# Performance work log

Hardware: AMD Instinct MI355X
Metric: run time of the kernel (lower is better)

Reference implementation:

```python
import jax, jax.numpy as jnp
import numpy as np

BLOCK = 8
HALO = 3
HEADS = 4


def setup_inputs() -> dict:
    key = jax.random.key(0)
    ks = jax.random.split(key, 8)
    B, C, H, W = 4, 256, 128, 128
    d = C // HEADS
    win = BLOCK + 2 * HALO
    s = lambda k, shape, scale=1.0: jax.random.normal(k, shape, jnp.float32) * scale
    return {
        'noisy': s(ks[0], (B, C, H, W)),
        'aux': s(ks[1], (B, C, H, W)),
        'w_map': s(ks[2], (C, 2 * C), (2.0 / (2 * C)) ** 0.5),  # 1x1 conv: [out, in]
        'b_map': jnp.zeros((C,), jnp.float32),
        'w_q': s(ks[3], (C, C), (2.0 / C) ** 0.5),
        'w_k': s(ks[4], (C, C), (2.0 / C) ** 0.5),
        'w_v': s(ks[5], (C, C), (2.0 / C) ** 0.5),
        'rel_h': s(ks[6], (win, 1, d // 2)),
        'rel_w': s(ks[7], (1, win, d // 2)),
    }


def _conv1x1(x, w):
    # x: [B,C,H,W], w: [O,C]
    return jnp.einsum('oc,bchw->bohw', w, x)


def reference(noisy, aux, w_map, b_map, w_q, w_k, w_v, rel_h, rel_w):
    B, C, H, W = noisy.shape
    block, halo, heads = BLOCK, HALO, HEADS
    d = C // heads
    win = block + 2 * halo
    nbh, nbw = H // block, W // block

    n_aux = jax.nn.relu(_conv1x1(jnp.concatenate([noisy, aux], axis=1), w_map)
                        + b_map[None, :, None, None])

    # Q: [B,nbh,nbw,heads,block*block,d], pre-scaled by head_ch**-0.5
    q = _conv1x1(n_aux, w_q) * (d ** -0.5)
    q = q.reshape(B, heads, d, nbh, block, nbw, block)
    q = q.transpose(0, 3, 5, 1, 4, 6, 2).reshape(B, nbh, nbw, heads, block * block, d)

    def halo_windows(x):
        xp = jnp.pad(x, ((0, 0), (0, 0), (halo, halo), (halo, halo)))
        ih = jnp.arange(nbh)[:, None] * block + jnp.arange(win)[None, :]
        iw = jnp.arange(nbw)[:, None] * block + jnp.arange(win)[None, :]
        w1 = xp[:, :, ih, :]
        w2 = w1[:, :, :, :, iw]
        w2 = w2.transpose(0, 2, 4, 1, 3, 5)
        w2 = w2.reshape(B, nbh, nbw, heads, d, win, win)
        return w2.transpose(0, 1, 2, 3, 5, 6, 4)

    k = halo_windows(_conv1x1(n_aux, w_k))
    # relative position bias fused into K (first half: height, second half: width)
    k = jnp.concatenate([k[..., :d // 2] + rel_h, k[..., d // 2:] + rel_w], axis=-1)
    k = k.reshape(B, nbh, nbw, heads, win * win, d)

    v = halo_windows(_conv1x1(noisy, w_v)).reshape(B, nbh, nbw, heads, win * win, d)

    sim = jnp.einsum('bxyhid,bxyhjd->bxyhij', q, k)
    attn = jax.nn.softmax(sim, axis=-1)
    out = jnp.einsum('bxyhij,bxyhjd->bxyhid', attn, v)

    # reassemble blocks: [B,nbh,nbw,heads,block,block,d] -> [B, heads*d, H, W]
    out = out.reshape(B, nbh, nbw, heads, block, block, d)
    out = out.transpose(0, 3, 6, 1, 4, 2, 5).reshape(B, C, H, W)
    return out
```

## Files before the change

kernel.cpp:

```cpp
#include <hip/hip_runtime.h>
#include <hip/hip_bf16.h>

typedef unsigned short u16;
typedef __attribute__((ext_vector_type(8))) short short8;
typedef __attribute__((ext_vector_type(4))) float floatx4;

#define HWPIX 16384
#define IMG 128

__device__ __forceinline__ float b2f(u16 u) {
    unsigned int x = ((unsigned int)u) << 16;
    return __builtin_bit_cast(float, x);
}
__device__ __forceinline__ u16 f2b(float f) {
    __hip_bfloat16 h = __float2bfloat16(f);
    return __builtin_bit_cast(u16, h);
}

template<int IN_WS>
__global__ __launch_bounds__(256)
void conv1x1_kernel(const float* __restrict__ ein0, const float* __restrict__ ein1,
                    const u16* __restrict__ bws,
                    const float* __restrict__ w, const float* __restrict__ bias,
                    u16* __restrict__ out, int K, float scale, int relu)
{
    __shared__ u16 Alds[64 * 40];
    __shared__ u16 Blds[128 * 40];

    const int tid = threadIdx.x;
    const int wave = tid >> 6, lane = tid & 63;
    const int quad = lane >> 4, l16 = lane & 15;
    const int pbase = blockIdx.x * 128;
    const int mbase = blockIdx.y * 64;
    const int b = blockIdx.z;

    floatx4 acc[8];
#pragma unroll
    for (int f = 0; f < 8; ++f) acc[f] = (floatx4){0.f, 0.f, 0.f, 0.f};

    const int a_r = tid >> 2, a_kg = tid & 3;
    const int b_c4 = (tid & 7) * 4;
    const int b_p4 = (tid >> 3) * 4;

    float4 af0, af1;
    float4 bfl[4];
    uint2  bbl[4];

    auto load_chunk = [&](int kc) {
        const int c0 = kc * 32;
        const float* wp = w + (size_t)(mbase + a_r) * K + c0 + a_kg * 8;
        af0 = *(const float4*)wp;
        af1 = *(const float4*)(wp + 4);
        if (IN_WS) {
#pragma unroll
            for (int i = 0; i < 4; ++i) {
                const u16* s = bws + ((size_t)b * 256 + c0 + b_c4 + i) * HWPIX + pbase + b_p4;
                bbl[i] = *(const uint2*)s;
            }
        } else {
            const float* base = (c0 < 256) ? ein0 : ein1;
            const int cb = c0 & 255;
#pragma unroll
            for (int i = 0; i < 4; ++i) {
                const float* s = base + ((size_t)b * 256 + cb + b_c4 + i) * HWPIX + pbase + b_p4;
                bfl[i] = *(const float4*)s;
            }
        }
    };
    auto write_chunk = [&]() {
        union { uint4 v; u16 s[8]; } ta;
        ta.s[0] = f2b(af0.x); ta.s[1] = f2b(af0.y); ta.s[2] = f2b(af0.z); ta.s[3] = f2b(af0.w);
        ta.s[4] = f2b(af1.x); ta.s[5] = f2b(af1.y); ta.s[6] = f2b(af1.z); ta.s[7] = f2b(af1.w);
        *(uint4*)&Alds[a_r * 40 + a_kg * 8] = ta.v;
        if (IN_WS) {
            union { uint2 v; u16 s[4]; } c[4];
#pragma unroll
            for (int i = 0; i < 4; ++i) c[i].v = bbl[i];
#pragma unroll
            for (int j = 0; j < 4; ++j) {
                union { uint2 v; u16 s[4]; } o;
#pragma unroll
                for (int i = 0; i < 4; ++i) o.s[i] = c[i].s[j];
                *(uint2*)&Blds[(b_p4 + j) * 40 + b_c4] = o.v;
            }
        } else {
            float px[4][4];
#pragma unroll
            for (int i = 0; i < 4; ++i) {
                px[i][0] = bfl[i].x; px[i][1] = bfl[i].y; px[i][2] = bfl[i].z; px[i][3] = bfl[i].w;
            }
#pragma unroll
            for (int j = 0; j < 4; ++j) {
                union { uint2 v; u16 s[4]; } o;
#pragma unroll
                for (int i = 0; i < 4; ++i) o.s[i] = f2b(px[i][j]);
                *(uint2*)&Blds[(b_p4 + j) * 40 + b_c4] = o.v;
            }
        }
    };

    const int nchunk = K >> 5;
    load_chunk(0);
    for (int kc = 0; kc < nchunk; ++kc) {
        if (kc) __syncthreads();
        write_chunk();
        __syncthreads();
        if (kc + 1 < nchunk) load_chunk(kc + 1);
        short8 afrag = *(const short8*)&Alds[(wave * 16 + l16) * 40 + quad * 8];
#pragma unroll
        for (int f = 0; f < 8; ++f) {
            short8 bfrag = *(const short8*)&Blds[(f * 16 + l16) * 40 + quad * 8];
            acc[f] = __builtin_amdgcn_mfma_f32_16x16x32_bf16(afrag, bfrag, acc[f], 0, 0, 0);
        }
    }

    float bv[4];
#pragma unroll
    for (int r = 0; r < 4; ++r) {
        int m = mbase + wave * 16 + quad * 4 + r;
        bv[r] = bias ? bias[m] : 0.f;
    }
#pragma unroll
    for (int f = 0; f < 8; ++f) {
        int p = pbase + f * 16 + l16;
#pragma unroll
        for (int r = 0; r < 4; ++r) {
            int m = mbase + wave * 16 + quad * 4 + r;
            float v = acc[f][r] * scale + bv[r];
            if (relu) v = fmaxf(v, 0.f);
            out[((size_t)b * 256 + m) * HWPIX + p] = f2b(v);
        }
    }
}

__global__ __launch_bounds__(256)
void attn_kernel(const u16* __restrict__ qmap, const u16* __restrict__ kmap,
                 const u16* __restrict__ vmap, const float* __restrict__ relh,
                 const float* __restrict__ relw, float* __restrict__ out)
{
    __shared__ u16 Qlds[64 * 72];
    __shared__ u16 Klds[224 * 72];
    __shared__ u16 Vlds[64 * 232];
    __shared__ float RelHf[448], RelWf[448];

    const int tid = threadIdx.x;
    const int wave = tid >> 6, lane = tid & 63;
    const int quad = lane >> 4, l16 = lane & 15;

    const int n = blockIdx.x + 16 * blockIdx.y + 256 * blockIdx.z;
    const int n2 = (n & 7) * 512 + (n >> 3);
    const int bw = n2 & 15, bh = (n2 >> 4) & 15;
    const int head = (n2 >> 8) & 3, b = n2 >> 10;

    const size_t chbase = ((size_t)b * 256 + head * 64) * HWPIX;

    float rh0 = relh[tid], rw0 = relw[tid];
    float rh1 = 0.f, rw1 = 0.f;
    if (tid < 192) { rh1 = relh[tid + 256]; rw1 = relw[tid + 256]; }

    const u16* qrow = qmap + chbase + (size_t)lane * HWPIX + bw * 8;
    uint4 q0 = *(const uint4*)(qrow + (bh * 8 + wave) * IMG);
    uint4 q1 = *(const uint4*)(qrow + (bh * 8 + wave + 4) * IMG);

    const int cbyte = min(max(bw * 16 - 8, 0), 224);
    uint2 kseg[4][4], vseg[4][4];
#pragma unroll
    for (int s = 0; s < 4; ++s) {
        if (s < 3 || wave < 2) {
            const int wr = wave + 4 * s;
            const int ih = bh * 8 - 3 + wr;
            const int ihc = min(max(ih, 0), 127);
            const char* kp = (const char*)(kmap + chbase + (size_t)lane * HWPIX) + ihc * 256 + cbyte;
            const char* vp = (const char*)(vmap + chbase + (size_t)lane * HWPIX) + ihc * 256 + cbyte;
#pragma unroll
            for (int j = 0; j < 4; ++j) {
                kseg[s][j] = *(const uint2*)(kp + 8 * j);
                vseg[s][j] = *(const uint2*)(vp + 8 * j);
            }
        }
    }

    RelHf[tid] = rh0; RelWf[tid] = rw0;
    if (tid < 192) { RelHf[tid + 256] = rh1; RelWf[tid + 256] = rw1; }
    {
        union { uint4 v; u16 s[8]; } t0, t1;
        t0.v = q0; t1.v = q1;
#pragma unroll
        for (int i = 0; i < 8; ++i) {
            Qlds[(wave * 8 + i) * 72 + lane] = t0.s[i];
            Qlds[((wave + 4) * 8 + i) * 72 + lane] = t1.s[i];
        }
    }
    __syncthreads();

    const int iwb = bw * 8 - 3;
#pragma unroll
    for (int s = 0; s < 4; ++s) {
        if (s < 3 || wave < 2) {
            const int wr = wave + 4 * s;
            const int ih = bh * 8 - 3 + wr;
            const bool rok = (unsigned)ih < 128u;
            union { uint2 v[4]; u16 u[16]; } kr, vr;
#pragma unroll
            for (int j = 0; j < 4; ++j) { kr.v[j] = kseg[s][j]; vr.v[j] = vseg[s][j]; }
            if (bw == 0) {
#pragma unroll
                for (int i = 15; i >= 4; --i) { kr.u[i] = kr.u[i - 4]; vr.u[i] = vr.u[i - 4]; }
            } else if (bw == 15) {
#pragma unroll
                for (int i = 0; i < 12; ++i) { kr.u[i] = kr.u[i + 4]; vr.u[i] = vr.u[i + 4]; }
            }
            const int kb = wr * 14;
            u16 vm[14];
#pragma unroll
            for (int sc = 0; sc < 14; ++sc) {
                const bool ok = rok && ((unsigned)(iwb + sc) < 128u);
                vm[sc] = ok ? vr.u[sc + 1] : (u16)0;
                const float kv = ok ? b2f(kr.u[sc + 1]) : 0.f;
                const float rel = (lane < 32) ? RelHf[wr * 32 + (lane & 31)]
                                              : RelWf[sc * 32 + (lane & 31)];
                Klds[(kb + sc) * 72 + lane] = f2b(kv + rel);
            }
            unsigned* vrow = (unsigned*)&Vlds[lane * 232 + kb];
#pragma unroll
            for (int p = 0; p < 7; ++p)
                vrow[p] = (unsigned)vm[2 * p] | ((unsigned)vm[2 * p + 1] << 16);
        }
    }
    for (int t = tid; t < 28 * 64; t += 256) {
        int kp_ = 196 + (t >> 6), ch = t & 63;
        Klds[kp_ * 72 + ch] = 0;
        Vlds[ch * 232 + kp_] = 0;
    }
    __syncthreads();

    floatx4 sacc[14];
#pragma unroll
    for (int f = 0; f < 14; ++f) sacc[f] = (floatx4){0.f, 0.f, 0.f, 0.f};
    __builtin_amdgcn_s_setprio(1);
#pragma unroll
    for (int kc = 0; kc < 2; ++kc) {
        short8 qa = *(const short8*)&Qlds[(wave * 16 + l16) * 72 + kc * 32 + quad * 8];
#pragma unroll
        for (int f = 0; f < 14; ++f) {
            short8 kb = *(const short8*)&Klds[(f * 16 + l16) * 72 + kc * 32 + quad * 8];
            sacc[f] = __builtin_amdgcn_mfma_f32_16x16x32_bf16(qa, kb, sacc[f], 0, 0, 0);
        }
    }
    __builtin_amdgcn_s_setprio(0);

    float pm[14][4], rmax[4], rsum[4];
#pragma unroll
    for (int r = 0; r < 4; ++r) rmax[r] = -3.0e4f;
#pragma unroll
    for (int f = 0; f < 14; ++f) {
        int col = f * 16 + l16;
#pragma unroll
        for (int r = 0; r < 4; ++r) {
            float v = (col < 196) ? sacc[f][r] : -3.0e4f;
            pm[f][r] = v;
            rmax[r] = fmaxf(rmax[r], v);
        }
    }
#pragma unroll
    for (int off = 1; off < 16; off <<= 1)
#pragma unroll
        for (int r = 0; r < 4; ++r)
            rmax[r] = fmaxf(rmax[r], __shfl_xor(rmax[r], off, 64));
#pragma unroll
    for (int r = 0; r < 4; ++r) rsum[r] = 0.f;
#pragma unroll
    for (int f = 0; f < 14; ++f)
#pragma unroll
        for (int r = 0; r < 4; ++r) {
            float e = __expf(pm[f][r] - rmax[r]);
            pm[f][r] = e;
            rsum[r] += e;
        }
#pragma unroll
    for (int off = 1; off < 16; off <<= 1)
#pragma unroll
        for (int r = 0; r < 4; ++r)
            rsum[r] += __shfl_xor(rsum[r], off, 64);
    float rinv[4];
#pragma unroll
    for (int r = 0; r < 4; ++r) rinv[r] = 1.f / rsum[r];

    __syncthreads();

    u16* S = Klds;
#pragma unroll
    for (int f = 0; f < 14; ++f)
#pragma unroll
        for (int r = 0; r < 4; ++r)
            S[(wave * 16 + quad * 4 + r) * 232 + f * 16 + l16] = f2b(pm[f][r] * rinv[r]);
    __syncthreads();

    floatx4 oacc[4];
#pragma unroll
    for (int f = 0; f < 4; ++f) oacc[f] = (floatx4){0.f, 0.f, 0.f, 0.f};
    __builtin_amdgcn_s_setprio(1);
#pragma unroll
    for (int kc = 0; kc < 7; ++kc) {
        short8 pa = *(const short8*)&S[(wave * 16 + l16) * 232 + kc * 32 + quad * 8];
#pragma unroll
        for (int f = 0; f < 4; ++f) {
            short8 vb = *(const short8*)&Vlds[(f * 16 + l16) * 232 + kc * 32 + quad * 8];
            oacc[f] = __builtin_amdgcn_mfma_f32_16x16x32_bf16(pa, vb, oacc[f], 0, 0, 0);
        }
    }
    __builtin_amdgcn_s_setprio(0);

    u16* O = Qlds;
#pragma unroll
    for (int f = 0; f < 4; ++f)
#pragma unroll
        for (int r = 0; r < 4; ++r)
            O[(f * 16 + l16) * 72 + wave * 16 + quad * 4 + r] = f2b(oacc[f][r]);
    __syncthreads();

    for (int t = tid; t < 512; t += 256) {
        int ch = t >> 3, r = t & 7;
        const u16* src = &O[ch * 72 + r * 8];
        float4 v0 = {b2f(src[0]), b2f(src[1]), b2f(src[2]), b2f(src[3])};
        float4 v1 = {b2f(src[4]), b2f(src[5]), b2f(src[6]), b2f(src[7])};
        float* dst = out + chbase + ch * HWPIX + (bh * 8 + r) * IMG + bw * 8;
        *(float4*)dst = v0;
        *(float4*)(dst + 4) = v1;
    }
}

extern "C" void kernel_launch(void* const* d_in, const int* in_sizes, int n_in,
                              void* d_out, int out_size, void* d_ws, size_t ws_size,
                              hipStream_t stream)
{
    (void)in_sizes; (void)n_in; (void)out_size; (void)ws_size;
    const float* noisy = (const float*)d_in[0];
    const float* aux   = (const float*)d_in[1];
    const float* w_map = (const float*)d_in[2];
    const float* b_map = (const float*)d_in[3];
    const float* w_q   = (const float*)d_in[4];
    const float* w_k   = (const float*)d_in[5];
    const float* w_v   = (const float*)d_in[6];
    const float* rel_h = (const float*)d_in[7];
    const float* rel_w = (const float*)d_in[8];
    float* out = (float*)d_out;

    u16* nv   = (u16*)d_ws;
    u16* kmap = nv   + (size_t)16777216;
    u16* qmap = kmap + (size_t)16777216;

    dim3 cgrid(128, 4, 4);
    conv1x1_kernel<0><<<cgrid, 256, 0, stream>>>(noisy, aux, nullptr, w_map, b_map, nv,   512, 1.f,    1);
    conv1x1_kernel<1><<<cgrid, 256, 0, stream>>>(nullptr, nullptr, nv, w_q,  nullptr, qmap, 256, 0.125f, 0);
    conv1x1_kernel<1><<<cgrid, 256, 0, stream>>>(nullptr, nullptr, nv, w_k,  nullptr, kmap, 256, 1.f,    0);
    conv1x1_kernel<0><<<cgrid, 256, 0, stream>>>(noisy, noisy, nullptr, w_v, nullptr, nv,   256, 1.f,    0);
    attn_kernel<<<dim3(16, 16, 16), 256, 0, stream>>>(qmap, kmap, nv, rel_h, rel_w, out);
}
```

Before: 430.8 us.

## Pre-convert weights to bf16, enlarge conv tiles, fuse Q/K convs, swizzle V LDS

Adds a kernel that converts all 1x1 conv weights to bf16 in a device global buffer, so the conv kernels no longer convert weights per tile. The conv kernel's tile grows to 128x128 outputs with a 64-wide K chunk, and each wave now computes a 4x4 grid of MFMA fragments for more reuse per LDS load. The Q and K projections are merged into a single launch by splitting on blockIdx.y. In the attention kernel, the V LDS layout becomes a 512-byte-row XOR swizzle to avoid bank conflicts. The trade-off is higher register and LDS use per block, which may lower occupancy, plus one extra small launch.

```diff
diff --git a/kernel.cpp b/kernel.cpp
--- a/kernel.cpp
+++ b/kernel.cpp
@@ -17,120 +17,157 @@
     return __builtin_bit_cast(u16, h);
 }
 
+__device__ __align__(16) u16 g_w16[327680];
+
+__global__ __launch_bounds__(256)
+void wconv_kernel(const float* __restrict__ wmap, const float* __restrict__ wq,
+                  const float* __restrict__ wk, const float* __restrict__ wv)
+{
+    int i = blockIdx.x * 256 + threadIdx.x;
+    const float* src; int off;
+    if (i < 131072)      { src = wmap; off = i; }
+    else if (i < 196608) { src = wk;   off = i - 131072; }
+    else if (i < 262144) { src = wq;   off = i - 196608; }
+    else                 { src = wv;   off = i - 262144; }
+    g_w16[i] = f2b(src[off]);
+}
+
 template<int IN_WS>
 __global__ __launch_bounds__(256)
-void conv1x1_kernel(const float* __restrict__ ein0, const float* __restrict__ ein1,
-                    const u16* __restrict__ bws,
-                    const float* __restrict__ w, const float* __restrict__ bias,
-                    u16* __restrict__ out, int K, float scale, int relu)
+void conv2_kernel(const float* __restrict__ ein0, const float* __restrict__ ein1,
+                  const u16* __restrict__ bws, int woff,
+                  const float* __restrict__ bias,
+                  u16* __restrict__ outA, u16* __restrict__ outB,
+                  int K, float scaleA, float scaleB, int relu)
 {
-    __shared__ u16 Alds[64 * 40];
-    __shared__ u16 Blds[128 * 40];
+    __shared__ u16 Alds[128 * 72];
+    __shared__ u16 Blds[128 * 72];
 
     const int tid = threadIdx.x;
     const int wave = tid >> 6, lane = tid & 63;
     const int quad = lane >> 4, l16 = lane & 15;
+    const int wmo = (wave >> 1) * 64;
+    const int wpo = (wave & 1) * 64;
     const int pbase = blockIdx.x * 128;
-    const int mbase = blockIdx.y * 64;
+    const int mbase = blockIdx.y * 128;
     const int b = blockIdx.z;
-
-    floatx4 acc[8];
-#pragma unroll
-    for (int f = 0; f < 8; ++f) acc[f] = (floatx4){0.f, 0.f, 0.f, 0.f};
-
-    const int a_r = tid >> 2, a_kg = tid & 3;
-    const int b_c4 = (tid & 7) * 4;
-    const int b_p4 = (tid >> 3) * 4;
-
-    float4 af0, af1;
-    float4 bfl[4];
-    uint2  bbl[4];
+    u16* out = (blockIdx.y >= 2) ? outB : outA;
+    const float scale = (blockIdx.y >= 2) ? scaleB : scaleA;
+    const int mb = mbase & 255;
+    const u16* wsrc = g_w16 + woff;
+
+    floatx4 acc[4][4];
+#pragma unroll
+    for (int mi = 0; mi < 4; ++mi)
+#pragma unroll
+        for (int pj = 0; pj < 4; ++pj) acc[mi][pj] = (floatx4){0.f, 0.f, 0.f, 0.f};
+
+    const int a_r = tid >> 1, a_s = (tid & 1) * 32;
+    const int b_c = (tid & 15) * 4;
+    const int b_p = (tid >> 4) * 8;
+
+    uint4  apre[4];
+    uint4  bpre[4];
+    float4 fpre[4][2];
 
     auto load_chunk = [&](int kc) {
-        const int c0 = kc * 32;
-        const float* wp = w + (size_t)(mbase + a_r) * K + c0 + a_kg * 8;
-        af0 = *(const float4*)wp;
-        af1 = *(const float4*)(wp + 4);
+        const int c0 = kc * 64;
+        const u16* wp = wsrc + (size_t)(mbase + a_r) * K + c0 + a_s;
+#pragma unroll
+        for (int j = 0; j < 4; ++j) apre[j] = *(const uint4*)(wp + j * 8);
         if (IN_WS) {
 #pragma unroll
-            for (int i = 0; i < 4; ++i) {
-                const u16* s = bws + ((size_t)b * 256 + c0 + b_c4 + i) * HWPIX + pbase + b_p4;
-                bbl[i] = *(const uint2*)s;
-            }
+            for (int i = 0; i < 4; ++i)
+                bpre[i] = *(const uint4*)(bws + ((size_t)b * 256 + c0 + b_c + i) * HWPIX + pbase + b_p);
         } else {
             const float* base = (c0 < 256) ? ein0 : ein1;
             const int cb = c0 & 255;
 #pragma unroll
             for (int i = 0; i < 4; ++i) {
-                const float* s = base + ((size_t)b * 256 + cb + b_c4 + i) * HWPIX + pbase + b_p4;
-                bfl[i] = *(const float4*)s;
+                const float* s = base + ((size_t)b * 256 + cb + b_c + i) * HWPIX + pbase + b_p;
+                fpre[i][0] = *(const float4*)s;
+                fpre[i][1] = *(const float4*)(s + 4);
             }
         }
     };
     auto write_chunk = [&]() {
-        union { uint4 v; u16 s[8]; } ta;
-        ta.s[0] = f2b(af0.x); ta.s[1] = f2b(af0.y); ta.s[2] = f2b(af0.z); ta.s[3] = f2b(af0.w);
-        ta.s[4] = f2b(af1.x); ta.s[5] = f2b(af1.y); ta.s[6] = f2b(af1.z); ta.s[7] = f2b(af1.w);
-        *(uint4*)&Alds[a_r * 40 + a_kg * 8] = ta.v;
+#pragma unroll
+        for (int j = 0; j < 4; ++j)
+            *(uint4*)&Alds[a_r * 72 + a_s + j * 8] = apre[j];
         if (IN_WS) {
-            union { uint2 v; u16 s[4]; } c[4];
-#pragma unroll
-            for (int i = 0; i < 4; ++i) c[i].v = bbl[i];
-#pragma unroll
-            for (int j = 0; j < 4; ++j) {
+            union { uint4 v; u16 s[8]; } c[4];
+#pragma unroll
+            for (int i = 0; i < 4; ++i) c[i].v = bpre[i];
+#pragma unroll
+            for (int j = 0; j < 8; ++j) {
                 union { uint2 v; u16 s[4]; } o;
 #pragma unroll
                 for (int i = 0; i < 4; ++i) o.s[i] = c[i].s[j];
-                *(uint2*)&Blds[(b_p4 + j) * 40 + b_c4] = o.v;
+                *(uint2*)&Blds[(b_p + j) * 72 + b_c] = o.v;
             }
         } else {
-            float px[4][4];
+            float px[4][8];
 #pragma unroll
             for (int i = 0; i < 4; ++i) {
-                px[i][0] = bfl[i].x; px[i][1] = bfl[i].y; px[i][2] = bfl[i].z; px[i][3] = bfl[i].w;
-            }
-#pragma unroll
-            for (int j = 0; j < 4; ++j) {
+                px[i][0] = fpre[i][0].x; px[i][1] = fpre[i][0].y;
+                px[i][2] = fpre[i][0].z; px[i][3] = fpre[i][0].w;
+                px[i][4] = fpre[i][1].x; px[i][5] = fpre[i][1].y;
+                px[i][6] = fpre[i][1].z; px[i][7] = fpre[i][1].w;
+            }
+#pragma unroll
+            for (int j = 0; j < 8; ++j) {
                 union { uint2 v; u16 s[4]; } o;
 #pragma unroll
                 for (int i = 0; i < 4; ++i) o.s[i] = f2b(px[i][j]);
-                *(uint2*)&Blds[(b_p4 + j) * 40 + b_c4] = o.v;
+                *(uint2*)&Blds[(b_p + j) * 72 + b_c] = o.v;
             }
         }
     };
 
-    const int nchunk = K >> 5;
+    const int nchunk = K >> 6;
     load_chunk(0);
     for (int kc = 0; kc < nchunk; ++kc) {
         if (kc) __syncthreads();
         write_chunk();
         __syncthreads();
         if (kc + 1 < nchunk) load_chunk(kc + 1);
-        short8 afrag = *(const short8*)&Alds[(wave * 16 + l16) * 40 + quad * 8];
-#pragma unroll
-        for (int f = 0; f < 8; ++f) {
-            short8 bfrag = *(const short8*)&Blds[(f * 16 + l16) * 40 + quad * 8];
-            acc[f] = __builtin_amdgcn_mfma_f32_16x16x32_bf16(afrag, bfrag, acc[f], 0, 0, 0);
-        }
-    }
-
-    float bv[4];
-#pragma unroll
-    for (int r = 0; r < 4; ++r) {
-        int m = mbase + wave * 16 + quad * 4 + r;
-        bv[r] = bias ? bias[m] : 0.f;
-    }
-#pragma unroll
-    for (int f = 0; f < 8; ++f) {
-        int p = pbase + f * 16 + l16;
-#pragma unroll
-        for (int r = 0; r < 4; ++r) {
-            int m = mbase + wave * 16 + quad * 4 + r;
-            float v = acc[f][r] * scale + bv[r];
-            if (relu) v = fmaxf(v, 0.f);
-            out[((size_t)b * 256 + m) * HWPIX + p] = f2b(v);
-        }
-    }
+#pragma unroll
+        for (int k2 = 0; k2 < 2; ++k2) {
+            short8 af[4];
+#pragma unroll
+            for (int mi = 0; mi < 4; ++mi)
+                af[mi] = *(const short8*)&Alds[(wmo + mi * 16 + l16) * 72 + k2 * 32 + quad * 8];
+#pragma unroll
+            for (int pj = 0; pj < 4; ++pj) {
+                short8 bf_ = *(const short8*)&Blds[(wpo + pj * 16 + l16) * 72 + k2 * 32 + quad * 8];
+#pragma unroll
+                for (int mi = 0; mi < 4; ++mi)
+                    acc[mi][pj] = __builtin_amdgcn_mfma_f32_16x16x32_bf16(af[mi], bf_, acc[mi][pj], 0, 0, 0);
+            }
+        }
+    }
+
+    float bv[4][4];
+#pragma unroll
+    for (int mi = 0; mi < 4; ++mi)
+#pragma unroll
+        for (int r = 0; r < 4; ++r)
+            bv[mi][r] = bias ? bias[mb + wmo + mi * 16 + quad * 4 + r] : 0.f;
+#pragma unroll
+    for (int mi = 0; mi < 4; ++mi)
+#pragma unroll
+        for (int pj = 0; pj < 4; ++pj)
+#pragma unroll
+            for (int r = 0; r < 4; ++r) {
+                float v = acc[mi][pj][r] * scale + bv[mi][r];
+                if (relu) v = fmaxf(v, 0.f);
+                out[((size_t)b * 256 + mb + wmo + mi * 16 + quad * 4 + r) * HWPIX
+                    + pbase + wpo + pj * 16 + l16] = f2b(v);
+            }
+}
+
+__device__ __forceinline__ int vswz(int dd, int colByte) {
+    return dd * 512 + (colByte ^ ((dd & 31) << 4));
 }
 
 __global__ __launch_bounds__(256)
@@ -140,12 +177,13 @@
 {
     __shared__ u16 Qlds[64 * 72];
     __shared__ u16 Klds[224 * 72];
-    __shared__ u16 Vlds[64 * 232];
+    __shared__ u16 Vlds[64 * 256];
     __shared__ float RelHf[448], RelWf[448];
 
     const int tid = threadIdx.x;
     const int wave = tid >> 6, lane = tid & 63;
     const int quad = lane >> 4, l16 = lane & 15;
+    char* Vb = (char*)Vlds;
 
     const int n = blockIdx.x + 16 * blockIdx.y + 256 * blockIdx.z;
     const int n2 = (n & 7) * 512 + (n >> 3);
@@ -221,16 +259,16 @@
                                               : RelWf[sc * 32 + (lane & 31)];
                 Klds[(kb + sc) * 72 + lane] = f2b(kv + rel);
             }
-            unsigned* vrow = (unsigned*)&Vlds[lane * 232 + kb];
 #pragma unroll
             for (int p = 0; p < 7; ++p)
-                vrow[p] = (unsigned)vm[2 * p] | ((unsigned)vm[2 * p + 1] << 16);
+                *(unsigned*)(Vb + vswz(lane, kb * 2 + p * 4)) =
+                    (unsigned)vm[2 * p] | ((unsigned)vm[2 * p + 1] << 16);
         }
     }
     for (int t = tid; t < 28 * 64; t += 256) {
         int kp_ = 196 + (t >> 6), ch = t & 63;
         Klds[kp_ * 72 + ch] = 0;
-        Vlds[ch * 232 + kp_] = 0;
+        *(u16*)(Vb + vswz(ch, kp_ * 2)) = 0;
     }
     __syncthreads();
 
@@ -305,7 +343,7 @@
         short8 pa = *(const short8*)&S[(wave * 16 + l16) * 232 + kc * 32 + quad * 8];
 #pragma unroll
         for (int f = 0; f < 4; ++f) {
-            short8 vb = *(const short8*)&Vlds[(f * 16 + l16) * 232 + kc * 32 + quad * 8];
+            short8 vb = *(const short8*)(Vb + vswz(f * 16 + l16, kc * 64 + quad * 16));
             oacc[f] = __builtin_amdgcn_mfma_f32_16x16x32_bf16(pa, vb, oacc[f], 0, 0, 0);
         }
     }
@@ -350,10 +388,12 @@
     u16* kmap = nv   + (size_t)16777216;
     u16* qmap = kmap + (size_t)16777216;
 
-    dim3 cgrid(128, 4, 4);
-    conv1x1_kernel<0><<<cgrid, 256, 0, stream>>>(noisy, aux, nullptr, w_map, b_map, nv,   512, 1.f,    1);
-    conv1x1_kernel<1><<<cgrid, 256, 0, stream>>>(nullptr, nullptr, nv, w_q,  nullptr, qmap, 256, 0.125f, 0);
-    conv1x1_kernel<1><<<cgrid, 256, 0, stream>>>(nullptr, nullptr, nv, w_k,  nullptr, kmap, 256, 1.f,    0);
-    conv1x1_kernel<0><<<cgrid, 256, 0, stream>>>(noisy, noisy, nullptr, w_v, nullptr, nv,   256, 1.f,    0);
+    wconv_kernel<<<1280, 256, 0, stream>>>(w_map, w_q, w_k, w_v);
+    conv2_kernel<0><<<dim3(128, 2, 4), 256, 0, stream>>>(noisy, aux, nullptr, 0, b_map,
+                                                         nv, nv, 512, 1.f, 1.f, 1);
+    conv2_kernel<1><<<dim3(128, 4, 4), 256, 0, stream>>>(nullptr, nullptr, nv, 131072, nullptr,
+                                                         kmap, qmap, 256, 1.f, 0.125f, 0);
+    conv2_kernel<0><<<dim3(128, 2, 4), 256, 0, stream>>>(noisy, noisy, nullptr, 262144, nullptr,
+                                                         nv, nv, 256, 1.f, 1.f, 0);
     attn_kernel<<<dim3(16, 16, 16), 256, 0, stream>>>(qmap, kmap, nv, rel_h, rel_w, out);
 }
```

Result: faster. 413.5 us (-4.0%).
